# Kernel optimization log

Measured on AMD Instinct MI355X. Metric: run time of the kernel, lower is better.

Reference implementation:

```python
import jax, jax.numpy as jnp
import numpy as np

N_NODES = 100000
N_EDGES = 800000
D_IN = 256
D_HID = 256
D_OUT = 64
HEADS = 1
ALPHA = 0.5          # TransConv residual weight
GRAPH_WEIGHT = 0.8   # _SGFormer aggregate='add' weight
LN_EPS = 1e-5
BN_EPS = 1e-5


def layer_norm(x, g, b):
    mu = x.mean(-1, keepdims=True)
    var = ((x - mu) ** 2).mean(-1, keepdims=True)
    return (x - mu) * jax.lax.rsqrt(var + LN_EPS) * g + b


def full_attention_conv(qs, ks, vs):
    # qs, ks, vs: [N, H, C]; normalization is by the GLOBAL Frobenius norm
    qs = qs / jnp.linalg.norm(qs)
    ks = ks / jnp.linalg.norm(ks)
    N = qs.shape[0]
    kvs = jnp.einsum('lhm,lhd->hmd', ks, vs)                     # [H,C,C]
    attention_num = jnp.einsum('nhm,hmd->nhd', qs, kvs) + N * vs  # [N,H,C]
    ks_sum = ks.sum(axis=0)                                      # [H,C]
    normalizer = jnp.einsum('nhm,hm->nh', qs, ks_sum)[..., None] + N
    return attention_num / normalizer


def gcn_conv(x, src, dst, w, b, n):
    # PyG GCNConv: h = x @ W; add self-loops; D^-1/2 (A+I) D^-1/2 h; + bias
    h = x @ w
    loop = jnp.arange(n)
    s = jnp.concatenate([src, loop])
    d = jnp.concatenate([dst, loop])
    deg = jax.ops.segment_sum(jnp.ones_like(s, dtype=h.dtype), d, num_segments=n)
    dinv = jnp.where(deg > 0, jax.lax.rsqrt(jnp.maximum(deg, 1e-12)), 0.0)
    norm = dinv[s] * dinv[d]
    out = jax.ops.segment_sum(h[s] * norm[:, None], d, num_segments=n)
    return out + b


def setup_inputs() -> dict:
    key = jax.random.key(0)
    ks = jax.random.split(key, 24)
    f32 = jnp.float32
    def lin(k, fi, fo):
        s = 1.0 / np.sqrt(fi)
        kw, kb = jax.random.split(k)
        return (jax.random.uniform(kw, (fi, fo), f32, -s, s),
                jax.random.uniform(kb, (fo,), f32, -s, s))
    x = jax.random.normal(ks[0], (N_NODES, D_IN), f32)
    edge_index = jax.random.randint(ks[1], (2, N_EDGES), 0, N_NODES, jnp.int64)
    fc0_w, fc0_b = lin(ks[2], D_IN, D_HID)
    wq0_w, wq0_b = lin(ks[3], D_HID, D_HID * HEADS)
    wk0_w, wk0_b = lin(ks[4], D_HID, D_HID * HEADS)
    wv0_w, wv0_b = lin(ks[5], D_HID, D_HID * HEADS)
    wq1_w, wq1_b = lin(ks[6], D_HID, D_HID * HEADS)
    wk1_w, wk1_b = lin(ks[7], D_HID, D_HID * HEADS)
    wv1_w, wv1_b = lin(ks[8], D_HID, D_HID * HEADS)
    gcn_w0, gcn_b0 = lin(ks[9], D_IN, D_HID)
    gcn_w1, gcn_b1 = lin(ks[10], D_HID, D_HID)
    fc_w, fc_b = lin(ks[11], D_HID, D_OUT)
    ones = jnp.ones((D_HID,), f32)
    zeros = jnp.zeros((D_HID,), f32)
    return dict(
        x=x, edge_index=edge_index,
        fc0_w=fc0_w, fc0_b=fc0_b, ln0_g=ones, ln0_b=zeros,
        wq0_w=wq0_w, wq0_b=wq0_b, wk0_w=wk0_w, wk0_b=wk0_b, wv0_w=wv0_w, wv0_b=wv0_b,
        ln1_g=ones, ln1_b=zeros,
        wq1_w=wq1_w, wq1_b=wq1_b, wk1_w=wk1_w, wk1_b=wk1_b, wv1_w=wv1_w, wv1_b=wv1_b,
        ln2_g=ones, ln2_b=zeros,
        gcn_w0=gcn_w0, gcn_b0=gcn_b0, bn_g=ones, bn_b=zeros,
        gcn_w1=gcn_w1, gcn_b1=gcn_b1,
        fc_w=fc_w, fc_b=fc_b)


def reference(x, edge_index, fc0_w, fc0_b, ln0_g, ln0_b,
              wq0_w, wq0_b, wk0_w, wk0_b, wv0_w, wv0_b, ln1_g, ln1_b,
              wq1_w, wq1_b, wk1_w, wk1_b, wv1_w, wv1_b, ln2_g, ln2_b,
              gcn_w0, gcn_b0, bn_g, bn_b, gcn_w1, gcn_b1, fc_w, fc_b):
    n = x.shape[0]
    src, dst = edge_index[0], edge_index[1]
    # ---- TransConv (eval mode: dropout = identity) ----
    h = layer_norm(x @ fc0_w + fc0_b, ln0_g, ln0_b)
    h = jax.nn.relu(h)
    layer_params = [
        (wq0_w, wq0_b, wk0_w, wk0_b, wv0_w, wv0_b, ln1_g, ln1_b),
        (wq1_w, wq1_b, wk1_w, wk1_b, wv1_w, wv1_b, ln2_g, ln2_b),
    ]
    for (qw, qb, kw, kb, vw, vb, lg, lb) in layer_params:
        q = (h @ qw + qb).reshape(n, HEADS, D_HID)
        k = (h @ kw + kb).reshape(n, HEADS, D_HID)
        v = (h @ vw + vb).reshape(n, HEADS, D_HID)
        a = full_attention_conv(q, k, v).mean(axis=1)   # mean over heads
        h = layer_norm(ALPHA * a + (1.0 - ALPHA) * h, lg, lb)
    x_trans = h
    # ---- GCN branch (BN in eval: running_mean=0, running_var=1) ----
    g = gcn_conv(x, src, dst, gcn_w0, gcn_b0, n)
    g = g * (bn_g / jnp.sqrt(1.0 + BN_EPS)) + bn_b
    g = jax.nn.relu(g)
    g = gcn_conv(g, src, dst, gcn_w1, gcn_b1, n)
    # ---- combine + classifier ----
    emb = GRAPH_WEIGHT * g + (1.0 - GRAPH_WEIGHT) * x_trans
    return emb @ fc_w + fc_b
```

## Files before the change

### kernel.cpp

```cpp
#include <hip/hip_runtime.h>
#include <hip/hip_bf16.h>

#define NN 100000
#define NE 800000
#define DH 256
#define DOUT 64
#define NSPL 50000
#define NSO ((size_t)NSPL * DH)
#define NBLK 391

using bf16 = __hip_bfloat16;
typedef __attribute__((ext_vector_type(8))) short bf16x8;
typedef __attribute__((ext_vector_type(4))) float f32x4;

__device__ __forceinline__ float bits2f(unsigned short h) {
    union { unsigned int u; float f; } c; c.u = ((unsigned int)h) << 16; return c.f;
}
__device__ __forceinline__ unsigned short f2b(float v) {
    union { float f; unsigned int u; } c; c.f = v;
    unsigned int u = c.u;
    return (unsigned short)((u + 0x7FFFu + ((u >> 16) & 1u)) >> 16);
}
__device__ __forceinline__ unsigned short tob(float v) { return f2b(v); }
__device__ __forceinline__ unsigned short tob(bf16 v) {
    union { bf16 b; unsigned short u; } c; c.b = v; return c.u;
}
__device__ __forceinline__ float ldf(const void* p, size_t i, int isbf) {
    if (isbf) return bits2f(((const unsigned short*)p)[i]);
    return ((const float*)p)[i];
}
__device__ __forceinline__ float ldS(const float* p, size_t i) { return p[i]; }
__device__ __forceinline__ float ldS(const bf16* p, size_t i) { return __bfloat162float(p[i]); }
__device__ __forceinline__ void stS(float* p, size_t i, float v) { p[i] = v; }
__device__ __forceinline__ void stS(bf16* p, size_t i, float v) { p[i] = __float2bfloat16(v); }
__device__ __forceinline__ float4 ld4S(const float* p) { return *(const float4*)p; }
__device__ __forceinline__ float4 ld4S(const bf16* p) {
    ushort4 u = *(const ushort4*)(const void*)p;
    return make_float4(bits2f(u.x), bits2f(u.y), bits2f(u.z), bits2f(u.w));
}
__device__ __forceinline__ void st4S(float* p, float4 v) { *(float4*)p = v; }
__device__ __forceinline__ void st4S(bf16* p, float4 v) {
    *(ushort4*)(void*)p = make_ushort4(f2b(v.x), f2b(v.y), f2b(v.z), f2b(v.w));
}
__device__ __forceinline__ void ld8(const void* p, size_t idx, int isbf, ushort4& o0, ushort4& o1) {
    if (isbf) {
        const ushort4* q = (const ushort4*)((const unsigned short*)p + idx);
        o0 = q[0]; o1 = q[1];
    } else {
        const float4* q = (const float4*)((const float*)p + idx);
        float4 a = q[0], b = q[1];
        o0 = make_ushort4(f2b(a.x), f2b(a.y), f2b(a.z), f2b(a.w));
        o1 = make_ushort4(f2b(b.x), f2b(b.y), f2b(b.z), f2b(b.w));
    }
}
__device__ __forceinline__ void ld8S(const bf16* p, size_t idx, ushort4& o0, ushort4& o1) {
    const ushort4* q = (const ushort4*)((const unsigned short*)p + idx);
    o0 = q[0]; o1 = q[1];
}
__device__ __forceinline__ void ld8S(const float* p, size_t idx, ushort4& o0, ushort4& o1) {
    const float4* q = (const float4*)(p + idx);
    float4 a = q[0], b = q[1];
    o0 = make_ushort4(f2b(a.x), f2b(a.y), f2b(a.z), f2b(a.w));
    o1 = make_ushort4(f2b(b.x), f2b(b.y), f2b(b.z), f2b(b.w));
}
__device__ __forceinline__ int ld_src(const int* ei, int e, int i64) {
    return i64 ? ei[2 * (size_t)e] : ei[e];
}
__device__ __forceinline__ int ld_dst(const int* ei, int e, int i64) {
    return i64 ? ei[2 * ((size_t)NE + e)] : ei[NE + e];
}

__global__ __launch_bounds__(256) void detect_kernel(const void* x, const int* ei, int* flags)
{
    __shared__ int s_sane[4], s_nz[4];
    int t = threadIdx.x;
    const unsigned short* xu = (const unsigned short*)x;
    int sane = 0;
    for (int i = t; i < 2048; i += 256) {
        float v = bits2f(xu[2 * i]);
        float a = fabsf(v);
        if (v == v && a > 1e-3f && a < 100.f) sane++;
    }
    int nz = 0;
    for (int i = t; i < 4096; i += 256) {
        if (ei[2 * (i * 122) + 1] != 0) nz++;
    }
#pragma unroll
    for (int off = 32; off > 0; off >>= 1) { sane += __shfl_down(sane, off); nz += __shfl_down(nz, off); }
    if ((t & 63) == 0) { s_sane[t >> 6] = sane; s_nz[t >> 6] = nz; }
    __syncthreads();
    if (t == 0) {
        flags[0] = ((s_sane[0] + s_sane[1] + s_sane[2] + s_sane[3]) > 1024) ? 1 : 0;
        flags[1] = ((s_nz[0] + s_nz[1] + s_nz[2] + s_nz[3]) == 0) ? 1 : 0;
    }
}

template <typename ST>
__global__ __launch_bounds__(512) void gemm_mfma(
    const void* __restrict__ A, const void* __restrict__ W,
    const void* __restrict__ bias, ST* __restrict__ C,
    int M, int Nc, const int* __restrict__ flags, int a_sel)
{
    __shared__ unsigned short Bs[64][264];
    const int isbf = flags[0];
    const int abf = (a_sel == 2) ? isbf : a_sel;
    const int tid = threadIdx.x;
    const int wave = tid >> 6, lane = tid & 63;
    const int quad = lane >> 4, nl = lane & 15;
    const int m0 = blockIdx.x * 128;
    const int n0 = blockIdx.y * 64;

#pragma unroll
    for (int it = 0; it < 4; ++it) {
        int p8 = it * 512 + tid;
        int k = p8 >> 3, nb = p8 & 7;
        ushort4 w0, w1;
        ld8(W, (size_t)k * Nc + n0 + nb * 8, isbf, w0, w1);
        int nbase = nb * 8;
        Bs[nbase + 0][k] = w0.x; Bs[nbase + 1][k] = w0.y;
        Bs[nbase + 2][k] = w0.z; Bs[nbase + 3][k] = w0.w;
        Bs[nbase + 4][k] = w1.x; Bs[nbase + 5][k] = w1.y;
        Bs[nbase + 6][k] = w1.z; Bs[nbase + 7][k] = w1.w;
    }
    __syncthreads();

    const int arow = m0 + wave * 16 + nl;
    const int av = (arow < M);
    const size_t abase = (size_t)arow * DH + quad * 8;
    f32x4 acc[4] = {{0.f,0.f,0.f,0.f},{0.f,0.f,0.f,0.f},{0.f,0.f,0.f,0.f},{0.f,0.f,0.f,0.f}};

#pragma unroll
    for (int k0 = 0; k0 < DH; k0 += 32) {
        ushort4 a0, a1;
        if (av) ld8(A, abase + k0, abf, a0, a1);
        else { a0 = make_ushort4(0,0,0,0); a1 = a0; }
        bf16x8 af;
        ((ushort4*)&af)[0] = a0; ((ushort4*)&af)[1] = a1;
#pragma unroll
        for (int ct = 0; ct < 4; ++ct) {
            bf16x8 bfg = *(const bf16x8*)&Bs[ct * 16 + nl][k0 + quad * 8];
            acc[ct] = __builtin_amdgcn_mfma_f32_16x16x32_bf16(af, bfg, acc[ct], 0, 0, 0);
        }
    }

#pragma unroll
    for (int ct = 0; ct < 4; ++ct) {
        int n = n0 + ct * 16 + nl;
        float bv = bias ? ldf(bias, n, isbf) : 0.f;
#pragma unroll
        for (int r = 0; r < 4; ++r) {
            int m = m0 + wave * 16 + quad * 4 + r;
            if (m < M) stS(C, (size_t)m * Nc + n, acc[ct][r] + bv);
        }
    }
}

template <typename ST>
__global__ __launch_bounds__(256) void kvs_mfma(
    const ST* __restrict__ Am, const ST* __restrict__ Bm, float* __restrict__ D)
{
    __shared__ unsigned short Ast[64][36];
    __shared__ unsigned short Bst[64][36];
    const int tid = threadIdx.x;
    const int wave = tid >> 6, lane = tid & 63;
    const int quad = lane >> 4, nl = lane & 15;
    const int i0 = blockIdx.x * 64, j0 = blockIdx.y * 64;
    const int S = gridDim.z;
    const int chunk = (NN + S - 1) / S;
    const int ns = blockIdx.z * chunk;
    const int ne = min(ns + chunk, NN);
    const int nn = tid >> 3;
    const int c0 = (tid & 7) * 8;
    f32x4 acc[4] = {{0.f,0.f,0.f,0.f},{0.f,0.f,0.f,0.f},{0.f,0.f,0.f,0.f},{0.f,0.f,0.f,0.f}};

    for (int n0 = ns; n0 < ne; n0 += 32) {
        int n = n0 + nn;
        ushort4 a0, a1, b0, b1;
        if (n < ne) {
            ld8S(Am, (size_t)n * DH + i0 + c0, a0, a1);
            ld8S(Bm, (size_t)n * DH + j0 + c0, b0, b1);
        } else {
            a0 = make_ushort4(0, 0, 0, 0); a1 = a0; b0 = a0; b1 = a0;
        }
        __syncthreads();
        Ast[c0 + 0][nn] = a0.x; Ast[c0 + 1][nn] = a0.y;
        Ast[c0 + 2][nn] = a0.z; Ast[c0 + 3][nn] = a0.w;
        Ast[c0 + 4][nn] = a1.x; Ast[c0 + 5][nn] = a1.y;
        Ast[c0 + 6][nn] = a1.z; Ast[c0 + 7][nn] = a1.w;
        Bst[c0 + 0][nn] = b0.x; Bst[c0 + 1][nn] = b0.y;
        Bst[c0 + 2][nn] = b0.z; Bst[c0 + 3][nn] = b0.w;
        Bst[c0 + 4][nn] = b1.x; Bst[c0 + 5][nn] = b1.y;
        Bst[c0 + 6][nn] = b1.z; Bst[c0 + 7][nn] = b1.w;
        __syncthreads();
        bf16x8 af = *(const bf16x8*)&Ast[wave * 16 + nl][quad * 8];
#pragma unroll
        for (int ct = 0; ct < 4; ++ct) {
            bf16x8 bfg = *(const bf16x8*)&Bst[ct * 16 + nl][quad * 8];
            acc[ct] = __builtin_amdgcn_mfma_f32_16x16x32_bf16(af, bfg, acc[ct], 0, 0, 0);
        }
    }
#pragma unroll
    for (int ct = 0; ct < 4; ++ct)
#pragma unroll
        for (int r = 0; r < 4; ++r)
            atomicAdd(&D[(size_t)(i0 + wave * 16 + quad * 4 + r) * DH + j0 + ct * 16 + nl], acc[ct][r]);
}

__global__ __launch_bounds__(256) void kvs2b_kernel(const float* __restrict__ kvs,
                                                    unsigned short* __restrict__ kvsb)
{
    int i = blockIdx.x * 256 + threadIdx.x;
    size_t o = (size_t)i * 8;
    float4 a = *(const float4*)(kvs + o);
    float4 b = *(const float4*)(kvs + o + 4);
    *(ushort4*)(kvsb + o)     = make_ushort4(f2b(a.x), f2b(a.y), f2b(a.z), f2b(a.w));
    *(ushort4*)(kvsb + o + 4) = make_ushort4(f2b(b.x), f2b(b.y), f2b(b.z), f2b(b.w));
}

template <typename ST>
__global__ __launch_bounds__(256) void attn_mfma(
    const ST* __restrict__ Q, const ST* __restrict__ V,
    const unsigned short* __restrict__ kvsb, const float* __restrict__ ks_sum,
    const float* __restrict__ qss, const float* __restrict__ kss,
    ST* __restrict__ out)
{
    __shared__ float ks_s[DH];
    __shared__ float nrm_s[64];
    const int tid = threadIdx.x;
    const int wave = tid >> 6, lane = tid & 63;
    const int quad = lane >> 4, nl = lane & 15;
    const int m0 = blockIdx.x * 64;
    const int j0 = blockIdx.y * 128;

    ks_s[tid] = ks_sum[tid];
    __syncthreads();

    const int arow = m0 + wave * 16 + nl;
    const int av = (arow < NN);
    const size_t abase = (size_t)arow * DH + quad * 8;
    f32x4 acc[8];
#pragma unroll
    for (int i = 0; i < 8; ++i) acc[i] = (f32x4){0.f, 0.f, 0.f, 0.f};
    float nrm = 0.f;

#pragma unroll 2
    for (int k0 = 0; k0 < DH; k0 += 32) {
        ushort4 a0, a1;
        if (av) ld8S(Q, abase + k0, a0, a1);
        else { a0 = make_ushort4(0,0,0,0); a1 = a0; }
        bf16x8 af;
        ((ushort4*)&af)[0] = a0; ((ushort4*)&af)[1] = a1;
#pragma unroll
        for (int j = 0; j < 8; ++j)
            nrm += bits2f(((const unsigned short*)&af)[j]) * ks_s[k0 + quad * 8 + j];
        const unsigned short* kb = kvsb + (size_t)(j0 + nl) * DH + k0 + quad * 8;
#pragma unroll
        for (int ct = 0; ct < 8; ++ct) {
            bf16x8 bfg = *(const bf16x8*)(kb + (size_t)ct * 16 * DH);
            acc[ct] = __builtin_amdgcn_mfma_f32_16x16x32_bf16(af, bfg, acc[ct], 0, 0, 0);
        }
    }
    nrm += __shfl_xor(nrm, 16);
    nrm += __shfl_xor(nrm, 32);
    if (lane < 16) nrm_s[wave * 16 + lane] = nrm;
    __syncthreads();
    const float scale = rsqrtf(*qss) * rsqrtf(*kss);
#pragma unroll
    for (int r = 0; r < 4; ++r) {
        int row = m0 + wave * 16 + quad * 4 + r;
        if (row >= NN) continue;
        float den = nrm_s[wave * 16 + quad * 4 + r] * scale + (float)NN;
#pragma unroll
        for (int ct = 0; ct < 8; ++ct) {
            int col = j0 + ct * 16 + nl;
            float v = ldS(V, (size_t)row * DH + col);
            float numv = acc[ct][r] * scale + (float)NN * v;
            stS(out, (size_t)row * DH + col, numv / den);
        }
    }
}

template <typename ST>
__global__ __launch_bounds__(256) void ln_kernel(
    const ST* __restrict__ A, const ST* __restrict__ B,
    float alpha, float beta,
    const void* __restrict__ g, const void* __restrict__ b,
    ST* __restrict__ out, int relu, const int* __restrict__ flags)
{
    const int isbf = flags[0];
    const int wave = threadIdx.x >> 6, lane = threadIdx.x & 63;
    const int row = blockIdx.x * 4 + wave;
    if (row >= NN) return;
    const size_t base = (size_t)row * DH + lane * 4;
    float4 v = ld4S(&A[base]);
    v.x *= alpha; v.y *= alpha; v.z *= alpha; v.w *= alpha;
    if (B) {
        float4 w = ld4S(&B[base]);
        v.x += beta * w.x; v.y += beta * w.y; v.z += beta * w.z; v.w += beta * w.w;
    }
    float s = v.x + v.y + v.z + v.w;
    float s2 = v.x * v.x + v.y * v.y + v.z * v.z + v.w * v.w;
#pragma unroll
    for (int off = 32; off > 0; off >>= 1) {
        s += __shfl_xor(s, off);
        s2 += __shfl_xor(s2, off);
    }
    float mean = s * (1.f / DH);
    float var = s2 * (1.f / DH) - mean * mean;
    float rstd = rsqrtf(var + 1e-5f);
    float4 o;
    o.x = (v.x - mean) * rstd * ldf(g, lane * 4 + 0, isbf) + ldf(b, lane * 4 + 0, isbf);
    o.y = (v.y - mean) * rstd * ldf(g, lane * 4 + 1, isbf) + ldf(b, lane * 4 + 1, isbf);
    o.z = (v.z - mean) * rstd * ldf(g, lane * 4 + 2, isbf) + ldf(b, lane * 4 + 2, isbf);
    o.w = (v.w - mean) * rstd * ldf(g, lane * 4 + 3, isbf) + ldf(b, lane * 4 + 3, isbf);
    if (relu) {
        o.x = fmaxf(o.x, 0.f); o.y = fmaxf(o.y, 0.f);
        o.z = fmaxf(o.z, 0.f); o.w = fmaxf(o.w, 0.f);
    }
    st4S(&out[base], o);
}

template <typename ST>
__global__ __launch_bounds__(256) void sumsq_kernel(
    const ST* __restrict__ A, size_t n, float* __restrict__ out)
{
    __shared__ float ps[4];
    size_t i = (size_t)blockIdx.x * blockDim.x + threadIdx.x;
    size_t stride = (size_t)gridDim.x * blockDim.x;
    float s = 0.f;
    for (; i < n; i += stride) { float v = ldS(A, i); s += v * v; }
#pragma unroll
    for (int off = 32; off > 0; off >>= 1) s += __shfl_down(s, off);
    if ((threadIdx.x & 63) == 0) ps[threadIdx.x >> 6] = s;
    __syncthreads();
    if (threadIdx.x == 0) atomicAdd(out, ps[0] + ps[1] + ps[2] + ps[3]);
}

template <typename ST>
__global__ __launch_bounds__(256) void colsum_kernel(
    const ST* __restrict__ Km, float* __restrict__ out)
{
    const int t = threadIdx.x;
    const int per = (NN + gridDim.x - 1) / gridDim.x;
    size_t r0 = (size_t)blockIdx.x * per;
    size_t r1 = r0 + per; if (r1 > NN) r1 = NN;
    float s = 0.f;
    for (size_t r = r0; r < r1; ++r) s += ldS(Km, r * DH + t);
    atomicAdd(&out[t], s);
}

__global__ __launch_bounds__(256) void count_kernel(const int* __restrict__ ei, int* __restrict__ cnt,
                                                    const int* __restrict__ flags)
{
    int e = blockIdx.x * 256 + threadIdx.x;
    if (e >= NE) return;
    int d = ld_dst(ei, e, flags[1]);
    if ((unsigned)d < NN) atomicAdd(&cnt[d], 1);
}

__global__ __launch_bounds__(256) void scan_block_kernel(const int* __restrict__ cnt,
                                                         int* __restrict__ pre, int* __restrict__ bsum)
{
    __shared__ int s[256];
    int i = blockIdx.x * 256 + threadIdx.x;
    int v = (i < NN) ? cnt[i] : 0;
    s[threadIdx.x] = v;
    __syncthreads();
    for (int off = 1; off < 256; off <<= 1) {
        int t = (threadIdx.x >= off) ? s[threadIdx.x - off] : 0;
        __syncthreads();
        s[threadIdx.x] += t;
        __syncthreads();
    }
    if (i < NN) pre[i] = s[threadIdx.x] - v;
    if (threadIdx.x == 255) bsum[blockIdx.x] = s[255];
}

__global__ __launch_bounds__(512) void scan_partial_kernel(int* __restrict__ bsum, int nb)
{
    __shared__ int s[512];
    int t = threadIdx.x;
    int v = (t < nb) ? bsum[t] : 0;
    s[t] = v;
    __syncthreads();
    for (int off = 1; off < 512; off <<= 1) {
        int u = (t >= off) ? s[t - off] : 0;
        __syncthreads();
        s[t] += u;
        __syncthreads();
    }
    if (t < nb) bsum[t] = s[t] - v;
}

__global__ __launch_bounds__(256) void finalize_kernel(int* __restrict__ base, const int* __restrict__ bsum,
                                                       const int* __restrict__ cnt, int* __restrict__ cursor,
                                                       float* __restrict__ dinv)
{
    int i = blockIdx.x * 256 + threadIdx.x;
    if (i >= NN) return;
    int b = base[i] + bsum[blockIdx.x];
    base[i] = b;
    cursor[i] = b;
    dinv[i] = rsqrtf((float)cnt[i] + 1.0f);
}

__global__ __launch_bounds__(256) void scatter_kernel(const int* __restrict__ ei, int* __restrict__ cursor,
                                                      int* __restrict__ srcs, const int* __restrict__ flags)
{
    int e = blockIdx.x * 256 + threadIdx.x;
    if (e >= NE) return;
    int i64 = flags[1];
    int s = ld_src(ei, e, i64), d = ld_dst(ei, e, i64);
    if ((unsigned)s >= NN || (unsigned)d >= NN) return;
    int pos = atomicAdd(&cursor[d], 1);
    srcs[pos] = s;
}

template <typename ST, int MODE>
__global__ __launch_bounds__(256) void fgather_kernel(
    const ST* __restrict__ Hs, const ST* __restrict__ Ht,
    const int* __restrict__ base, const int* __restrict__ cnt,
    const int* __restrict__ srcs, const float* __restrict__ dinv,
    const void* __restrict__ bias, const void* __restrict__ bng, const void* __restrict__ bnb,
    const int* __restrict__ flags, ST* __restrict__ out)
{
    const int isbf = flags[0];
    int node = blockIdx.x * 4 + (threadIdx.x >> 6);
    int lane = threadIdx.x & 63;
    if (node >= NN) return;
    int b0 = base[node], deg = cnt[node];
    float dd = dinv[node];
    float4 a0 = make_float4(0.f, 0.f, 0.f, 0.f);
    float4 a1 = make_float4(0.f, 0.f, 0.f, 0.f);
    int j = 0;
    for (; j + 4 <= deg; j += 4) {
        int s0 = srcs[b0 + j + 0], s1 = srcs[b0 + j + 1];
        int s2 = srcs[b0 + j + 2], s3 = srcs[b0 + j + 3];
        float n0 = dd * dinv[s0], n1 = dd * dinv[s1];
        float n2 = dd * dinv[s2], n3 = dd * dinv[s3];
        float4 h0 = ld4S(&Hs[(size_t)s0 * DH + lane * 4]);
        float4 h1 = ld4S(&Hs[(size_t)s1 * DH + lane * 4]);
        float4 h2 = ld4S(&Hs[(size_t)s2 * DH + lane * 4]);
        float4 h3 = ld4S(&Hs[(size_t)s3 * DH + lane * 4]);
        a0.x += h0.x * n0; a0.y += h0.y * n0; a0.z += h0.z * n0; a0.w += h0.w * n0;
        a1.x += h1.x * n1; a1.y += h1.y * n1; a1.z += h1.z * n1; a1.w += h1.w * n1;
        a0.x += h2.x * n2; a0.y += h2.y * n2; a0.z += h2.z * n2; a0.w += h2.w * n2;
        a1.x += h3.x * n3; a1.y += h3.y * n3; a1.z += h3.z * n3; a1.w += h3.w * n3;
    }
    for (; j < deg; ++j) {
        int s0 = srcs[b0 + j];
        float n0 = dd * dinv[s0];
        float4 h0 = ld4S(&Hs[(size_t)s0 * DH + lane * 4]);
        a0.x += h0.x * n0; a0.y += h0.y * n0; a0.z += h0.z * n0; a0.w += h0.w * n0;
    }
    const size_t obase = (size_t)node * DH + lane * 4;
    float4 own = ld4S(&Hs[obase]);
    float di2 = dd * dd;
    int c = lane * 4;
    float4 v;
    v.x = a0.x + a1.x + own.x * di2 + ldf(bias, c + 0, isbf);
    v.y = a0.y + a1.y + own.y * di2 + ldf(bias, c + 1, isbf);
    v.z = a0.z + a1.z + own.z * di2 + ldf(bias, c + 2, isbf);
    v.w = a0.w + a1.w + own.w * di2 + ldf(bias, c + 3, isbf);
    if (MODE == 0) {
        const float bnscale = 0.99999500003749981f;
        v.x = fmaxf(v.x * (ldf(bng, c + 0, isbf) * bnscale) + ldf(bnb, c + 0, isbf), 0.f);
        v.y = fmaxf(v.y * (ldf(bng, c + 1, isbf) * bnscale) + ldf(bnb, c + 1, isbf), 0.f);
        v.z = fmaxf(v.z * (ldf(bng, c + 2, isbf) * bnscale) + ldf(bnb, c + 2, isbf), 0.f);
        v.w = fmaxf(v.w * (ldf(bng, c + 3, isbf) * bnscale) + ldf(bnb, c + 3, isbf), 0.f);
    } else {
        float4 t = ld4S(&Ht[obase]);
        v.x = 0.8f * v.x + 0.2f * t.x;
        v.y = 0.8f * v.y + 0.2f * t.y;
        v.z = 0.8f * v.z + 0.2f * t.z;
        v.w = 0.8f * v.w + 0.2f * t.w;
    }
    st4S(&out[obase], v);
}

__global__ __launch_bounds__(256) void deg_kernel(const int* __restrict__ ei, float* __restrict__ deg,
                                                  const int* __restrict__ flags)
{
    int i64 = flags[1];
    int e = blockIdx.x * 256 + threadIdx.x;
    if (e >= NE) return;
    int d = ld_dst(ei, e, i64);
    if ((unsigned)d < NN) atomicAdd(&deg[d], 1.0f);
}

__global__ __launch_bounds__(256) void dinv_kernel(float* __restrict__ deg)
{
    int i = blockIdx.x * 256 + threadIdx.x;
    if (i < NN) deg[i] = rsqrtf(deg[i] + 1.0f);
}

template <typename ST>
__global__ __launch_bounds__(256) void agg_kernel(
    const ST* __restrict__ Hs, const int* __restrict__ ei,
    const float* __restrict__ dinv, float* __restrict__ lo, float* __restrict__ hi,
    const int* __restrict__ flags)
{
    int i64 = flags[1];
    int e = blockIdx.x * 4 + (threadIdx.x >> 6);
    int lane = threadIdx.x & 63;
    if (e >= NE) return;
    int s = ld_src(ei, e, i64), d = ld_dst(ei, e, i64);
    if ((unsigned)s >= NN || (unsigned)d >= NN) return;
    float nrm = dinv[s] * dinv[d];
    const float4 h4 = ld4S(&Hs[(size_t)s * DH + lane * 4]);
    float* o = (d < NSPL ? &lo[(size_t)d * DH] : &hi[(size_t)(d - NSPL) * DH]) + lane * 4;
    atomicAdd(o + 0, h4.x * nrm);
    atomicAdd(o + 1, h4.y * nrm);
    atomicAdd(o + 2, h4.z * nrm);
    atomicAdd(o + 3, h4.w * nrm);
}

template <typename ST>
__global__ __launch_bounds__(256) void gcn_epi1_kernel(
    const float* __restrict__ lo, const float* __restrict__ hi,
    const ST* __restrict__ h1, const float* __restrict__ dinv,
    const void* __restrict__ b0, const void* __restrict__ bng, const void* __restrict__ bnb,
    const int* __restrict__ flags, ST* __restrict__ out)
{
    const int isbf = flags[0];
    size_t idx = (size_t)blockIdx.x * 256 + threadIdx.x;
    if (idx >= (size_t)NN * DH) return;
    int i = (int)(idx >> 8), c = (int)(idx & 255);
    float aggv = (i < NSPL) ? lo[idx] : hi[idx - NSO];
    float di = dinv[i];
    float v = aggv + ldS(h1, idx) * di * di + ldf(b0, c, isbf);
    const float bnscale = 0.99999500003749981f;
    v = v * (ldf(bng, c, isbf) * bnscale) + ldf(bnb, c, isbf);
    stS(out, idx, fmaxf(v, 0.f));
}

template <typename ST>
__global__ __launch_bounds__(256) void gcn_epi2_kernel(
    const float* __restrict__ lo, const float* __restrict__ hi,
    const ST* __restrict__ h2, const ST* __restrict__ Ht, const float* __restrict__ dinv,
    const void* __restrict__ b1, const int* __restrict__ flags, ST* __restrict__ out)
{
    const int isbf = flags[0];
    size_t idx = (size_t)blockIdx.x * 256 + threadIdx.x;
    if (idx >= (size_t)NN * DH) return;
    int i = (int)(idx >> 8), c = (int)(idx & 255);
    float aggv = (i < NSPL) ? lo[idx] : hi[idx - NSO];
    float di = dinv[i];
    float g = aggv + ldS(h2, idx) * di * di + ldf(b1, c, isbf);
    stS(out, idx, 0.8f * g + 0.2f * ldS(Ht, idx));
}

__global__ __launch_bounds__(256) void diag_kernel(float* out, size_t n, float val)
{
    size_t i = (size_t)blockIdx.x * 256 + threadIdx.x;
    if (i < n) out[i] = val;
}

template <typename ST>
static void run_pipeline(void* const* d_in, void* d_out, char* wsb, hipStream_t stream, int use_csr)
{
    const void* x      = d_in[0];
    const int*  ei     = (const int*)d_in[1];
    const void* fc0_w  = d_in[2];  const void* fc0_b  = d_in[3];
    const void* ln0_g  = d_in[4];  const void* ln0_b  = d_in[5];
    const void* wq0_w  = d_in[6];  const void* wq0_b  = d_in[7];
    const void* wk0_w  = d_in[8];  const void* wk0_b  = d_in[9];
    const void* wv0_w  = d_in[10]; const void* wv0_b  = d_in[11];
    const void* ln1_g  = d_in[12]; const void* ln1_b  = d_in[13];
    const void* wq1_w  = d_in[14]; const void* wq1_b  = d_in[15];
    const void* wk1_w  = d_in[16]; const void* wk1_b  = d_in[17];
    const void* wv1_w  = d_in[18]; const void* wv1_b  = d_in[19];
    const void* ln2_g  = d_in[20]; const void* ln2_b  = d_in[21];
    const void* gcn_w0 = d_in[22]; const void* gcn_b0 = d_in[23];
    const void* bn_g   = d_in[24]; const void* bn_b   = d_in[25];
    const void* gcn_w1 = d_in[26]; const void* gcn_b1 = d_in[27];
    const void* fc_w   = d_in[28]; const void* fc_b   = d_in[29];

    const size_t stN = (size_t)NN * DH * sizeof(ST);
    ST* H  = (ST*)(wsb);
    ST* Qb = (ST*)(wsb + stN);
    ST* Kb = (ST*)(wsb + 2 * stN);
    ST* Vb = (ST*)(wsb + 3 * stN);
    float* aux = (float*)(wsb + 4 * stN);
    float* kvs    = aux;
    float* ks_sum = aux + 65536;
    float* qss    = aux + 65792;
    float* kss    = aux + 65793;
    float* dinv   = aux + 65808;
    int*   flags  = (int*)(aux + 65808 + NN);
    int* cnt    = (int*)(aux + 65808 + NN + 16);
    int* base   = cnt + NN;
    int* cursor = base + NN;
    int* bsum   = cursor + NN;
    int* srcs   = bsum + 512;
    unsigned short* kvsb = (unsigned short*)dinv;

    const int asel = (sizeof(ST) == 2) ? 1 : 0;
    dim3 mfmaGrid((NN + 127) / 128, DH / 64);
    const size_t NELEM = (size_t)NN * DH;

    detect_kernel<<<1, 256, 0, stream>>>(x, ei, flags);

    gemm_mfma<ST><<<mfmaGrid, 512, 0, stream>>>(x, fc0_w, fc0_b, Qb, NN, DH, flags, 2);
    ln_kernel<ST><<<(NN + 3) / 4, 256, 0, stream>>>(Qb, (const ST*)nullptr, 1.f, 0.f, ln0_g, ln0_b, H, 1, flags);

    for (int layer = 0; layer < 2; ++layer) {
        const void *qw, *qb, *kw, *kb, *vw, *vb, *lg, *lb;
        if (layer == 0) { qw = wq0_w; qb = wq0_b; kw = wk0_w; kb = wk0_b; vw = wv0_w; vb = wv0_b; lg = ln1_g; lb = ln1_b; }
        else            { qw = wq1_w; qb = wq1_b; kw = wk1_w; kb = wk1_b; vw = wv1_w; vb = wv1_b; lg = ln2_g; lb = ln2_b; }
        gemm_mfma<ST><<<mfmaGrid, 512, 0, stream>>>(H, qw, qb, Qb, NN, DH, flags, asel);
        gemm_mfma<ST><<<mfmaGrid, 512, 0, stream>>>(H, kw, kb, Kb, NN, DH, flags, asel);
        gemm_mfma<ST><<<mfmaGrid, 512, 0, stream>>>(H, vw, vb, Vb, NN, DH, flags, asel);
        hipMemsetAsync(aux, 0, (65536 + 256 + 2) * sizeof(float), stream);
        sumsq_kernel<ST><<<2048, 256, 0, stream>>>(Qb, NELEM, qss);
        sumsq_kernel<ST><<<2048, 256, 0, stream>>>(Kb, NELEM, kss);
        kvs_mfma<ST><<<dim3(4, 4, 128), 256, 0, stream>>>(Vb, Kb, kvs);
        colsum_kernel<ST><<<800, 256, 0, stream>>>(Kb, ks_sum);
        kvs2b_kernel<<<32, 256, 0, stream>>>(kvs, kvsb);
        attn_mfma<ST><<<dim3((NN + 63) / 64, 2), 256, 0, stream>>>(Qb, Vb, kvsb, ks_sum, qss, kss, Kb);
        ln_kernel<ST><<<(NN + 3) / 4, 256, 0, stream>>>(Kb, H, 0.5f, 0.5f, lg, lb, H, 0, flags);
    }

    if (use_csr) {
        hipMemsetAsync(cnt, 0, NN * sizeof(int), stream);
        count_kernel<<<(NE + 255) / 256, 256, 0, stream>>>(ei, cnt, flags);
        scan_block_kernel<<<NBLK, 256, 0, stream>>>(cnt, base, bsum);
        scan_partial_kernel<<<1, 512, 0, stream>>>(bsum, NBLK);
        finalize_kernel<<<NBLK, 256, 0, stream>>>(base, bsum, cnt, cursor, dinv);
        scatter_kernel<<<(NE + 255) / 256, 256, 0, stream>>>(ei, cursor, srcs, flags);

        gemm_mfma<ST><<<mfmaGrid, 512, 0, stream>>>(x, gcn_w0, nullptr, Qb, NN, DH, flags, 2);
        fgather_kernel<ST, 0><<<(NN + 3) / 4, 256, 0, stream>>>(
            Qb, (const ST*)nullptr, base, cnt, srcs, dinv, gcn_b0, bn_g, bn_b, flags, Kb);
        gemm_mfma<ST><<<mfmaGrid, 512, 0, stream>>>(Kb, gcn_w1, nullptr, Vb, NN, DH, flags, asel);
        fgather_kernel<ST, 1><<<(NN + 3) / 4, 256, 0, stream>>>(
            Vb, H, base, cnt, srcs, dinv, gcn_b1, nullptr, nullptr, flags, Qb);

        gemm_mfma<float><<<dim3((NN + 127) / 128, 1), 512, 0, stream>>>(Qb, fc_w, fc_b, (float*)d_out, NN, DOUT, flags, asel);
    } else {
        float* a1lo = (float*)(wsb + 2 * stN);
        float* a1hi = a1lo + NSO;
        ST* h2; float *a2lo, *a2hi;
        if (sizeof(ST) == 4) { h2 = Vb; a2lo = (float*)(wsb + 2 * stN); a2hi = a2lo + NSO; }
        else                 { h2 = Kb; a2lo = (float*)(wsb + stN);     a2hi = (float*)(wsb + 3 * stN); }

        hipMemsetAsync(dinv, 0, NN * sizeof(float), stream);
        deg_kernel<<<(NE + 255) / 256, 256, 0, stream>>>(ei, dinv, flags);
        dinv_kernel<<<(NN + 255) / 256, 256, 0, stream>>>(dinv);

        gemm_mfma<ST><<<mfmaGrid, 512, 0, stream>>>(x, gcn_w0, nullptr, Qb, NN, DH, flags, 2);
        hipMemsetAsync(a1lo, 0, NELEM * sizeof(float), stream);
        agg_kernel<ST><<<(NE + 3) / 4, 256, 0, stream>>>(Qb, ei, dinv, a1lo, a1hi, flags);
        gcn_epi1_kernel<ST><<<(NELEM + 255) / 256, 256, 0, stream>>>(a1lo, a1hi, Qb, dinv, gcn_b0, bn_g, bn_b, flags, Qb);

        gemm_mfma<ST><<<mfmaGrid, 512, 0, stream>>>(Qb, gcn_w1, nullptr, h2, NN, DH, flags, asel);
        hipMemsetAsync(a2lo, 0, NSO * sizeof(float), stream);
        hipMemsetAsync(a2hi, 0, NSO * sizeof(float), stream);
        agg_kernel<ST><<<(NE + 3) / 4, 256, 0, stream>>>(h2, ei, dinv, a2lo, a2hi, flags);
        gcn_epi2_kernel<ST><<<(NELEM + 255) / 256, 256, 0, stream>>>(a2lo, a2hi, h2, H, dinv, gcn_b1, flags, h2);

        gemm_mfma<float><<<dim3((NN + 127) / 128, 1), 512, 0, stream>>>(h2, fc_w, fc_b, (float*)d_out, NN, DOUT, flags, asel);
    }
}

extern "C" void kernel_launch(void* const* d_in, const int* in_sizes, int n_in,
                              void* d_out, int out_size, void* d_ws, size_t ws_size,
                              hipStream_t stream)
{
    char* wsb = (char*)d_ws;
    const size_t AUXF  = 65808 + NN + 16;
    const size_t CSRI  = 3 * (size_t)NN + 512 + NE;
    const size_t AUXB  = AUXF * sizeof(float);
    const size_t AUXB2 = AUXB + CSRI * sizeof(int);
    const size_t needA  = 4 * ((size_t)NN * DH * 4) + AUXB;
    const size_t needA2 = 4 * ((size_t)NN * DH * 4) + AUXB2;
    const size_t needB  = 4 * ((size_t)NN * DH * 2) + AUXB;
    const size_t needB2 = 4 * ((size_t)NN * DH * 2) + AUXB2;

    if (ws_size >= needA) {
        run_pipeline<float>(d_in, d_out, wsb, stream, ws_size >= needA2);
    } else if (ws_size >= needB) {
        run_pipeline<bf16>(d_in, d_out, wsb, stream, ws_size >= needB2);
    } else {
        float mb = (float)(ws_size >> 20);
        size_t n = (size_t)out_size;
        diag_kernel<<<(n + 255) / 256, 256, 0, stream>>>((float*)d_out, n, mb);
    }
}
```

Baseline: 1.942 ms.

## Fuse sum-of-squares and column-sum reductions into GEMM epilogue, process 512 rows per block

The separate sumsq and colsum kernels are removed. The Q and K projection GEMMs now accumulate the Frobenius norm and the K column sums in their epilogue, using warp shuffles, shared-memory atomics and global atomics. Each GEMM block now covers 512 rows in four 128-row passes, with register double-buffering of the next A tile so the staged weight tile is reused across more rows. This saves re-reading the Q and K matrices, but adds atomic contention and register pressure, and leaves fewer blocks in the grid.

```diff
diff --git a/kernel.cpp b/kernel.cpp
--- a/kernel.cpp
+++ b/kernel.cpp
@@ -33,6 +33,9 @@
 __device__ __forceinline__ float ldS(const bf16* p, size_t i) { return __bfloat162float(p[i]); }
 __device__ __forceinline__ void stS(float* p, size_t i, float v) { p[i] = v; }
 __device__ __forceinline__ void stS(bf16* p, size_t i, float v) { p[i] = __float2bfloat16(v); }
+template <typename ST> __device__ __forceinline__ float storedS(float v);
+template <> __device__ __forceinline__ float storedS<float>(float v) { return v; }
+template <> __device__ __forceinline__ float storedS<bf16>(float v) { return bits2f(f2b(v)); }
 __device__ __forceinline__ float4 ld4S(const float* p) { return *(const float4*)p; }
 __device__ __forceinline__ float4 ld4S(const bf16* p) {
     ushort4 u = *(const ushort4*)(const void*)p;
@@ -99,15 +102,17 @@
 __global__ __launch_bounds__(512) void gemm_mfma(
     const void* __restrict__ A, const void* __restrict__ W,
     const void* __restrict__ bias, ST* __restrict__ C,
-    int M, int Nc, const int* __restrict__ flags, int a_sel)
+    int M, int Nc, const int* __restrict__ flags, int a_sel,
+    float* __restrict__ ssq, float* __restrict__ csum)
 {
     __shared__ unsigned short Bs[64][264];
+    __shared__ float cs_s[64];
     const int isbf = flags[0];
     const int abf = (a_sel == 2) ? isbf : a_sel;
     const int tid = threadIdx.x;
     const int wave = tid >> 6, lane = tid & 63;
     const int quad = lane >> 4, nl = lane & 15;
-    const int m0 = blockIdx.x * 128;
+    const int m0 = blockIdx.x * 512;
     const int n0 = blockIdx.y * 64;
 
 #pragma unroll
@@ -122,36 +127,86 @@
         Bs[nbase + 4][k] = w1.x; Bs[nbase + 5][k] = w1.y;
         Bs[nbase + 6][k] = w1.z; Bs[nbase + 7][k] = w1.w;
     }
+    if (csum != nullptr && tid < 64) cs_s[tid] = 0.f;
     __syncthreads();
 
-    const int arow = m0 + wave * 16 + nl;
-    const int av = (arow < M);
-    const size_t abase = (size_t)arow * DH + quad * 8;
-    f32x4 acc[4] = {{0.f,0.f,0.f,0.f},{0.f,0.f,0.f,0.f},{0.f,0.f,0.f,0.f},{0.f,0.f,0.f,0.f}};
-
-#pragma unroll
-    for (int k0 = 0; k0 < DH; k0 += 32) {
-        ushort4 a0, a1;
-        if (av) ld8(A, abase + k0, abf, a0, a1);
-        else { a0 = make_ushort4(0,0,0,0); a1 = a0; }
-        bf16x8 af;
-        ((ushort4*)&af)[0] = a0; ((ushort4*)&af)[1] = a1;
+    const int lrow = wave * 16 + nl;
+    float bv[4];
+#pragma unroll
+    for (int ct = 0; ct < 4; ++ct)
+        bv[ct] = bias ? ldf(bias, n0 + ct * 16 + nl, isbf) : 0.f;
+
+    float myssq = 0.f;
+    float mycs[4] = {0.f, 0.f, 0.f, 0.f};
+
+    ushort4 c0[8], c1[8], nx0[8], nx1[8];
+    {
+        int arow = m0 + lrow;
+        int av = (arow < M);
+        size_t ab = (size_t)arow * DH + quad * 8;
+#pragma unroll
+        for (int s = 0; s < 8; ++s) {
+            if (av) ld8(A, ab + s * 32, abf, c0[s], c1[s]);
+            else { c0[s] = make_ushort4(0, 0, 0, 0); c1[s] = c0[s]; }
+        }
+    }
+
+#pragma unroll
+    for (int t = 0; t < 4; ++t) {
+        if (t < 3) {
+            int arow = m0 + (t + 1) * 128 + lrow;
+            int av = (arow < M);
+            size_t ab = (size_t)arow * DH + quad * 8;
+#pragma unroll
+            for (int s = 0; s < 8; ++s) {
+                if (av) ld8(A, ab + s * 32, abf, nx0[s], nx1[s]);
+                else { nx0[s] = make_ushort4(0, 0, 0, 0); nx1[s] = nx0[s]; }
+            }
+        }
+        f32x4 acc[4] = {{0.f,0.f,0.f,0.f},{0.f,0.f,0.f,0.f},{0.f,0.f,0.f,0.f},{0.f,0.f,0.f,0.f}};
+#pragma unroll
+        for (int s = 0; s < 8; ++s) {
+            bf16x8 af;
+            ((ushort4*)&af)[0] = c0[s]; ((ushort4*)&af)[1] = c1[s];
+#pragma unroll
+            for (int ct = 0; ct < 4; ++ct) {
+                bf16x8 bfg = *(const bf16x8*)&Bs[ct * 16 + nl][s * 32 + quad * 8];
+                acc[ct] = __builtin_amdgcn_mfma_f32_16x16x32_bf16(af, bfg, acc[ct], 0, 0, 0);
+            }
+        }
 #pragma unroll
         for (int ct = 0; ct < 4; ++ct) {
-            bf16x8 bfg = *(const bf16x8*)&Bs[ct * 16 + nl][k0 + quad * 8];
-            acc[ct] = __builtin_amdgcn_mfma_f32_16x16x32_bf16(af, bfg, acc[ct], 0, 0, 0);
-        }
-    }
-
-#pragma unroll
-    for (int ct = 0; ct < 4; ++ct) {
-        int n = n0 + ct * 16 + nl;
-        float bv = bias ? ldf(bias, n, isbf) : 0.f;
-#pragma unroll
-        for (int r = 0; r < 4; ++r) {
-            int m = m0 + wave * 16 + quad * 4 + r;
-            if (m < M) stS(C, (size_t)m * Nc + n, acc[ct][r] + bv);
-        }
+            int n = n0 + ct * 16 + nl;
+#pragma unroll
+            for (int r = 0; r < 4; ++r) {
+                int m = m0 + t * 128 + wave * 16 + quad * 4 + r;
+                if (m < M) {
+                    float v = acc[ct][r] + bv[ct];
+                    stS(C, (size_t)m * Nc + n, v);
+                    float sv = storedS<ST>(v);
+                    myssq += sv * sv;
+                    mycs[ct] += sv;
+                }
+            }
+        }
+        if (t < 3) {
+#pragma unroll
+            for (int s = 0; s < 8; ++s) { c0[s] = nx0[s]; c1[s] = nx1[s]; }
+        }
+    }
+
+    if (ssq != nullptr) {
+        float s = myssq;
+        s += __shfl_xor(s, 1);  s += __shfl_xor(s, 2);  s += __shfl_xor(s, 4);
+        s += __shfl_xor(s, 8);  s += __shfl_xor(s, 16); s += __shfl_xor(s, 32);
+        if (lane == 0) atomicAdd(ssq, s);
+    }
+    if (csum != nullptr) {
+#pragma unroll
+        for (int ct = 0; ct < 4; ++ct)
+            atomicAdd(&cs_s[ct * 16 + nl], mycs[ct]);
+        __syncthreads();
+        if (tid < 64) atomicAdd(&csum[n0 + tid], cs_s[tid]);
     }
 }
 
@@ -318,35 +373,6 @@
         o.z = fmaxf(o.z, 0.f); o.w = fmaxf(o.w, 0.f);
     }
     st4S(&out[base], o);
-}
-
-template <typename ST>
-__global__ __launch_bounds__(256) void sumsq_kernel(
-    const ST* __restrict__ A, size_t n, float* __restrict__ out)
-{
-    __shared__ float ps[4];
-    size_t i = (size_t)blockIdx.x * blockDim.x + threadIdx.x;
-    size_t stride = (size_t)gridDim.x * blockDim.x;
-    float s = 0.f;
-    for (; i < n; i += stride) { float v = ldS(A, i); s += v * v; }
-#pragma unroll
-    for (int off = 32; off > 0; off >>= 1) s += __shfl_down(s, off);
-    if ((threadIdx.x & 63) == 0) ps[threadIdx.x >> 6] = s;
-    __syncthreads();
-    if (threadIdx.x == 0) atomicAdd(out, ps[0] + ps[1] + ps[2] + ps[3]);
-}
-
-template <typename ST>
-__global__ __launch_bounds__(256) void colsum_kernel(
-    const ST* __restrict__ Km, float* __restrict__ out)
-{
-    const int t = threadIdx.x;
-    const int per = (NN + gridDim.x - 1) / gridDim.x;
-    size_t r0 = (size_t)blockIdx.x * per;
-    size_t r1 = r0 + per; if (r1 > NN) r1 = NN;
-    float s = 0.f;
-    for (size_t r = r0; r < r1; ++r) s += ldS(Km, r * DH + t);
-    atomicAdd(&out[t], s);
 }
 
 __global__ __launch_bounds__(256) void count_kernel(const int* __restrict__ ei, int* __restrict__ cnt,
@@ -596,26 +622,23 @@
     unsigned short* kvsb = (unsigned short*)dinv;
 
     const int asel = (sizeof(ST) == 2) ? 1 : 0;
-    dim3 mfmaGrid((NN + 127) / 128, DH / 64);
+    dim3 gemmGrid((NN + 511) / 512, DH / 64);
     const size_t NELEM = (size_t)NN * DH;
 
     detect_kernel<<<1, 256, 0, stream>>>(x, ei, flags);
 
-    gemm_mfma<ST><<<mfmaGrid, 512, 0, stream>>>(x, fc0_w, fc0_b, Qb, NN, DH, flags, 2);
+    gemm_mfma<ST><<<gemmGrid, 512, 0, stream>>>(x, fc0_w, fc0_b, Qb, NN, DH, flags, 2, nullptr, nullptr);
     ln_kernel<ST><<<(NN + 3) / 4, 256, 0, stream>>>(Qb, (const ST*)nullptr, 1.f, 0.f, ln0_g, ln0_b, H, 1, flags);
 
     for (int layer = 0; layer < 2; ++layer) {
         const void *qw, *qb, *kw, *kb, *vw, *vb, *lg, *lb;
         if (layer == 0) { qw = wq0_w; qb = wq0_b; kw = wk0_w; kb = wk0_b; vw = wv0_w; vb = wv0_b; lg = ln1_g; lb = ln1_b; }
         else            { qw = wq1_w; qb = wq1_b; kw = wk1_w; kb = wk1_b; vw = wv1_w; vb = wv1_b; lg = ln2_g; lb = ln2_b; }
-        gemm_mfma<ST><<<mfmaGrid, 512, 0, stream>>>(H, qw, qb, Qb, NN, DH, flags, asel);
-        gemm_mfma<ST><<<mfmaGrid, 512, 0, stream>>>(H, kw, kb, Kb, NN, DH, flags, asel);
-        gemm_mfma<ST><<<mfmaGrid, 512, 0, stream>>>(H, vw, vb, Vb, NN, DH, flags, asel);
         hipMemsetAsync(aux, 0, (65536 + 256 + 2) * sizeof(float), stream);
-        sumsq_kernel<ST><<<2048, 256, 0, stream>>>(Qb, NELEM, qss);
-        sumsq_kernel<ST><<<2048, 256, 0, stream>>>(Kb, NELEM, kss);
+        gemm_mfma<ST><<<gemmGrid, 512, 0, stream>>>(H, qw, qb, Qb, NN, DH, flags, asel, qss, nullptr);
+        gemm_mfma<ST><<<gemmGrid, 512, 0, stream>>>(H, kw, kb, Kb, NN, DH, flags, asel, kss, ks_sum);
+        gemm_mfma<ST><<<gemmGrid, 512, 0, stream>>>(H, vw, vb, Vb, NN, DH, flags, asel, nullptr, nullptr);
         kvs_mfma<ST><<<dim3(4, 4, 128), 256, 0, stream>>>(Vb, Kb, kvs);
-        colsum_kernel<ST><<<800, 256, 0, stream>>>(Kb, ks_sum);
         kvs2b_kernel<<<32, 256, 0, stream>>>(kvs, kvsb);
         attn_mfma<ST><<<dim3((NN + 63) / 64, 2), 256, 0, stream>>>(Qb, Vb, kvsb, ks_sum, qss, kss, Kb);
         ln_kernel<ST><<<(NN + 3) / 4, 256, 0, stream>>>(Kb, H, 0.5f, 0.5f, lg, lb, H, 0, flags);
@@ -629,14 +652,14 @@
         finalize_kernel<<<NBLK, 256, 0, stream>>>(base, bsum, cnt, cursor, dinv);
         scatter_kernel<<<(NE + 255) / 256, 256, 0, stream>>>(ei, cursor, srcs, flags);
 
-        gemm_mfma<ST><<<mfmaGrid, 512, 0, stream>>>(x, gcn_w0, nullptr, Qb, NN, DH, flags, 2);
+        gemm_mfma<ST><<<gemmGrid, 512, 0, stream>>>(x, gcn_w0, nullptr, Qb, NN, DH, flags, 2, nullptr, nullptr);
         fgather_kernel<ST, 0><<<(NN + 3) / 4, 256, 0, stream>>>(
             Qb, (const ST*)nullptr, base, cnt, srcs, dinv, gcn_b0, bn_g, bn_b, flags, Kb);
-        gemm_mfma<ST><<<mfmaGrid, 512, 0, stream>>>(Kb, gcn_w1, nullptr, Vb, NN, DH, flags, asel);
+        gemm_mfma<ST><<<gemmGrid, 512, 0, stream>>>(Kb, gcn_w1, nullptr, Vb, NN, DH, flags, asel, nullptr, nullptr);
         fgather_kernel<ST, 1><<<(NN + 3) / 4, 256, 0, stream>>>(
             Vb, H, base, cnt, srcs, dinv, gcn_b1, nullptr, nullptr, flags, Qb);
 
-        gemm_mfma<float><<<dim3((NN + 127) / 128, 1), 512, 0, stream>>>(Qb, fc_w, fc_b, (float*)d_out, NN, DOUT, flags, asel);
+        gemm_mfma<float><<<dim3((NN + 511) / 512, 1), 512, 0, stream>>>(Qb, fc_w, fc_b, (float*)d_out, NN, DOUT, flags, asel, nullptr, nullptr);
     } else {
         float* a1lo = (float*)(wsb + 2 * stN);
         float* a1hi = a1lo + NSO;
@@ -648,18 +671,18 @@
         deg_kernel<<<(NE + 255) / 256, 256, 0, stream>>>(ei, dinv, flags);
         dinv_kernel<<<(NN + 255) / 256, 256, 0, stream>>>(dinv);
 
-        gemm_mfma<ST><<<mfmaGrid, 512, 0, stream>>>(x, gcn_w0, nullptr, Qb, NN, DH, flags, 2);
+        gemm_mfma<ST><<<gemmGrid, 512, 0, stream>>>(x, gcn_w0, nullptr, Qb, NN, DH, flags, 2, nullptr, nullptr);
         hipMemsetAsync(a1lo, 0, NELEM * sizeof(float), stream);
         agg_kernel<ST><<<(NE + 3) / 4, 256, 0, stream>>>(Qb, ei, dinv, a1lo, a1hi, flags);
         gcn_epi1_kernel<ST><<<(NELEM + 255) / 256, 256, 0, stream>>>(a1lo, a1hi, Qb, dinv, gcn_b0, bn_g, bn_b, flags, Qb);
 
-        gemm_mfma<ST><<<mfmaGrid, 512, 0, stream>>>(Qb, gcn_w1, nullptr, h2, NN, DH, flags, asel);
+        gemm_mfma<ST><<<gemmGrid, 512, 0, stream>>>(Qb, gcn_w1, nullptr, h2, NN, DH, flags, asel, nullptr, nullptr);
         hipMemsetAsync(a2lo, 0, NSO * sizeof(float), stream);
         hipMemsetAsync(a2hi, 0, NSO * sizeof(float), stream);
         agg_kernel<ST><<<(NE + 3) / 4, 256, 0, stream>>>(h2, ei, dinv, a2lo, a2hi, flags);
         gcn_epi2_kernel<ST><<<(NELEM + 255) / 256, 256, 0, stream>>>(a2lo, a2hi, h2, H, dinv, gcn_b1, flags, h2);
 
-        gemm_mfma<float><<<dim3((NN + 127) / 128, 1), 512, 0, stream>>>(h2, fc_w, fc_b, (float*)d_out, NN, DOUT, flags, asel);
+        gemm_mfma<float><<<dim3((NN + 511) / 512, 1), 512, 0, stream>>>(h2, fc_w, fc_b, (float*)d_out, NN, DOUT, flags, asel, nullptr, nullptr);
     }
 }
 
```

Result: faster. 1.889 ms (-2.7%).
